# Kernel optimization log

Measured on AMD Instinct MI355X. Metric: run time of the kernel, lower is better.

The kernel has to match this reference:

```python
import jax, jax.numpy as jnp
import numpy as np

# SparseSphereConv (graph_level=6 -> V=40962, kernel_size=9, stride=1, select_index=None)
# Pipeline: neighbor gather -> data-dependent nonzero row selection ->
# per-vertex KxK interpolation matmul -> 1xK conv (linear over C_in,K) -> scatter back.
# With stride=1 / select_index=None the static selection is the identity, so the
# dynamic nonzero selection is equivalent to computing all rows and zeroing the
# rows whose gathered features are entirely zero (selected rows are scattered back,
# unselected rows stay 0 in sparse_reset's zero-initialized output).

BS, C_IN, C_OUT, V, K = 4, 32, 32, 40962, 9

def setup_inputs() -> dict:
    key = jax.random.key(0)
    k1, k2, k3, k4, k5 = jax.random.split(key, 5)
    x = jax.random.normal(k1, (BS, C_IN, V), dtype=jnp.float32)
    index = jax.random.randint(k2, (V, K), 0, V, dtype=jnp.int32)          # neighbor ids per vertex
    itp_mat = jax.random.uniform(k3, (V, K, K), dtype=jnp.float32)         # per-vertex interpolation
    conv_w = jax.random.normal(k4, (C_OUT, C_IN, K), dtype=jnp.float32) * 0.05  # Conv2d(C_in,C_out,(1,K)) weight
    conv_b = jax.random.normal(k5, (C_OUT,), dtype=jnp.float32) * 0.05
    return {"x": x, "index": index, "itp_mat": itp_mat, "conv_w": conv_w, "conv_b": conv_b}

def reference(x, index, itp_mat, conv_w, conv_b):
    # x: [bs, C, V] -> permute(2,0,1) -> gather neighbors -> [V, K, bs, C]
    g = jnp.transpose(x, (2, 0, 1))[index]
    g = jnp.transpose(g, (3, 2, 0, 1))                      # [C, bs, V, K]  (== reshape of [C, bs*V, K])
    # sparse_prepare: keep rows whose min or max over (C, K) is nonzero (detached in torch)
    gd = jax.lax.stop_gradient(g)
    rmin = gd.min(axis=(0, 3))                              # [bs, V]
    rmax = gd.max(axis=(0, 3))                              # [bs, V]
    mask = (rmin != 0) | (rmax != 0)                        # [bs, V]
    # Interploate: [C, S, 1, K] @ [S, K, K] per row -> batched small matmul
    interp = jnp.einsum('cbvk,vkj->cbvj', g, itp_mat)       # [C, bs, V, K]
    # Conv2d with kernel (1, K): contraction over (C_in, K) + bias
    out = jnp.einsum('cbvk,ock->bov', interp, conv_w) + conv_b[None, :, None]  # [bs, C_out, V]
    # sparse_reset: rows not selected stay zero
    return out * mask[:, None, :].astype(out.dtype)
```

## Files before the change

kernel.cpp:

```cpp
#include <hip/hip_runtime.h>
#include <hip/hip_bf16.h>

#define NV 40962
#define NK 9
#define CIN 32
#define COUT 32
#define NT 2561
#define NV81 (NV * 81)
#define NV9  (NV * 9)

typedef __attribute__((ext_vector_type(8))) short bf16x8;
typedef __attribute__((ext_vector_type(4))) float f32x4;
typedef __attribute__((ext_vector_type(2))) float f32x2;

#define PKFMA_L(A, G, R) asm("v_pk_fma_f32 %0, %1, %2, %0 op_sel:[0,0,0] op_sel_hi:[0,1,1]" : "+v"(A) : "v"(G), "v"(R))
#define PKFMA_H(A, G, R) asm("v_pk_fma_f32 %0, %1, %2, %0 op_sel:[1,0,0] op_sel_hi:[1,1,1]" : "+v"(A) : "v"(G), "v"(R))
#define PKMUL_L(A, G, R) asm("v_pk_mul_f32 %0, %1, %2 op_sel:[0,0] op_sel_hi:[0,1]" : "=v"(A) : "v"(G), "v"(R))
#define PKMUL_H(A, G, R) asm("v_pk_mul_f32 %0, %1, %2 op_sel:[1,0] op_sel_hi:[1,1]" : "=v"(A) : "v"(G), "v"(R))

#define ACC(cc, j) ((j) == 8 ? acc8[cc] : (((j) & 1) ? acc2[cc][(j) >> 1].y \
                                                     : acc2[cc][(j) >> 1].x))

__device__ __forceinline__ unsigned pkbf(float a, float b) {
    union { __hip_bfloat162 h2; unsigned u; } cv;
    cv.h2 = __float22bfloat162_rn(make_float2(a, b));
    return cv.u;
}

__global__ void __launch_bounds__(256) transpose_x_bf16(
    const float* __restrict__ x, unsigned* __restrict__ xtw,
    const float* __restrict__ w, unsigned short* __restrict__ wbf)
{
    __shared__ unsigned U[64 * 65];
    const int t = threadIdx.x;

    const int ci = blockIdx.x * 256 + t;
    if (ci < COUT * CIN * NK) {
        const int o = ci / 288;
        const int r = ci - o * 288;
        const int c = r / 9;
        const int j = r - c * 9;
        unsigned u = __float_as_uint(w[ci]);
        wbf[o * 288 + j * 32 + c] =
            (unsigned short)((u + 0x7FFFu + ((u >> 16) & 1u)) >> 16);
    }

    const int v0  = blockIdx.x * 64;
    const int l16 = t & 15;
    const int p   = t >> 4;

    #pragma unroll
    for (int i = 0; i < 4; ++i) {
        const int q    = p * 4 + i;
        const int r0   = 2 * q;
        const int bb   = r0 >> 5;
        const int c0   = r0 & 31;
        const int dwb  = (c0 >> 3) * 16 + bb * 4 + ((c0 & 7) >> 1);
        const float* rowA = x + (size_t)r0 * NV + v0;
        const float* rowB = rowA + NV;
        #pragma unroll
        for (int hv = 0; hv < 2; ++hv) {
            const int v = l16 * 2 + hv * 32;
            float2 a = make_float2(0.f, 0.f), c2 = make_float2(0.f, 0.f);
            if (v0 + v < NV) {
                a  = *(const float2*)(rowA + v);
                c2 = *(const float2*)(rowB + v);
            }
            U[(v    ) * 65 + dwb] = pkbf(a.x, c2.x);
            U[(v + 1) * 65 + dwb] = pkbf(a.y, c2.y);
        }
    }
    __syncthreads();

    const int v  = t >> 2;
    const int qo = t & 3;
    if (v0 + v < NV) {
        #pragma unroll
        for (int j = 0; j < 4; ++j) {
            const int n = j * 4 + qo;
            uint4 d;
            d.x = U[v * 65 + n * 4 + 0];
            d.y = U[v * 65 + n * 4 + 1];
            d.z = U[v * 65 + n * 4 + 2];
            d.w = U[v * 65 + n * 4 + 3];
            *(uint4*)&xtw[(size_t)(v0 + v) * 64 + n * 4] = d;
        }
    }
}

__global__ void __launch_bounds__(256, 2) sparse_conv_mfma(
    const unsigned short* __restrict__ xt, const int* __restrict__ index,
    const float* __restrict__ itp, const unsigned short* __restrict__ wbf,
    const float* __restrict__ bias, float* __restrict__ out)
{
    __shared__ float itp_s[4][4][108];

    const int t    = threadIdx.x;
    const int w    = t >> 6;
    const int lane = t & 63;
    const int arow = lane & 15;
    const int coct = lane >> 4;
    const int b    = (lane >> 2) & 3;
    const int vv   = lane & 3;
    const int tile = blockIdx.x;

    int ia = tile * 144 + w * 36 + (lane < 36 ? lane : 35);
    ia = ia < NV9 ? ia : NV9 - 1;
    const int myidx = index[ia];

    float iv[6];
    const size_t ibase = (size_t)(tile * 16 + w * 4) * 81;
    #pragma unroll
    for (int i = 0; i < 6; ++i) {
        const int o = i * 64 + lane;
        iv[i] = (o < 324 && ibase + o < (size_t)NV81) ? itp[ibase + o] : 0.0f;
    }

    const unsigned short* wb0 = wbf + arow * 288 + coct * 8;
    uint4 wa0[NK], wa1[NK];
    #pragma unroll
    for (int ks = 0; ks < NK; ++ks) {
        wa0[ks] = *(const uint4*)(wb0 + ks * 32);
        wa1[ks] = *(const uint4*)(wb0 + 16 * 288 + ks * 32);
    }

    float bs0[4], bs1[4];
    #pragma unroll
    for (int r = 0; r < 4; ++r) {
        bs0[r] = bias[coct * 4 + r];
        bs1[r] = bias[coct * 4 + 16 + r];
    }

    int nbr[NK];
    #pragma unroll
    for (int n = 0; n < NK; ++n) nbr[n] = __shfl(myidx, vv * 9 + n);
    const unsigned short* gbase = xt + coct * 32 + b * 8;
    uint4 g[NK];
    #pragma unroll
    for (int n = 0; n < NK; ++n)
        g[n] = *(const uint4*)(gbase + (size_t)nbr[n] * 128);

    #pragma unroll
    for (int i = 0; i < 6; ++i) {
        const int o = i * 64 + lane;
        if (o < 324) {
            const int vloc = o / 81;
            const int r2   = o - vloc * 81;
            const int kk   = r2 / 9;
            const int jj   = r2 - kk * 9;
            itp_s[w][vloc][kk * 12 + jj] = iv[i];
        }
    }
    __builtin_amdgcn_wave_barrier();

    unsigned frag[9][4];
    unsigned nzbits = 0;
    #pragma unroll
    for (int n = 0; n < NK; ++n)
        nzbits |= (g[n].x | g[n].y | g[n].z | g[n].w);
    nzbits &= 0x7FFF7FFFu;

    const float* ib = &itp_s[w][vv][0];
    #pragma unroll
    for (int h = 0; h < 2; ++h) {
        f32x2 acc2[4][4];
        float acc8[4];
        #pragma unroll
        for (int n = 0; n < NK; ++n) {
            const uint2 gk = h ? make_uint2(g[n].z, g[n].w)
                               : make_uint2(g[n].x, g[n].y);
            f32x2 gp01, gp23;
            gp01.x = __uint_as_float(gk.x << 16);
            gp01.y = __uint_as_float(gk.x & 0xFFFF0000u);
            gp23.x = __uint_as_float(gk.y << 16);
            gp23.y = __uint_as_float(gk.y & 0xFFFF0000u);
            const float* ir = ib + n * 12;
            const f32x4 ra = *(const f32x4*)ir;
            const f32x4 rb = *(const f32x4*)(ir + 4);
            const float r8 = ir[8];
            f32x2 rp[4];
            rp[0] = __builtin_shufflevector(ra, ra, 0, 1);
            rp[1] = __builtin_shufflevector(ra, ra, 2, 3);
            rp[2] = __builtin_shufflevector(rb, rb, 0, 1);
            rp[3] = __builtin_shufflevector(rb, rb, 2, 3);
            if (n == 0) {
                #pragma unroll
                for (int jp = 0; jp < 4; ++jp) {
                    PKMUL_L(acc2[0][jp], gp01, rp[jp]);
                    PKMUL_H(acc2[1][jp], gp01, rp[jp]);
                    PKMUL_L(acc2[2][jp], gp23, rp[jp]);
                    PKMUL_H(acc2[3][jp], gp23, rp[jp]);
                }
                acc8[0] = gp01.x * r8; acc8[1] = gp01.y * r8;
                acc8[2] = gp23.x * r8; acc8[3] = gp23.y * r8;
            } else {
                #pragma unroll
                for (int jp = 0; jp < 4; ++jp) {
                    PKFMA_L(acc2[0][jp], gp01, rp[jp]);
                    PKFMA_H(acc2[1][jp], gp01, rp[jp]);
                    PKFMA_L(acc2[2][jp], gp23, rp[jp]);
                    PKFMA_H(acc2[3][jp], gp23, rp[jp]);
                }
                acc8[0] += gp01.x * r8; acc8[1] += gp01.y * r8;
                acc8[2] += gp23.x * r8; acc8[3] += gp23.y * r8;
            }
        }
        #pragma unroll
        for (int ks = 0; ks < 9; ++ks) {
            frag[ks][2 * h]     = pkbf(ACC(0, ks), ACC(1, ks));
            frag[ks][2 * h + 1] = pkbf(ACC(2, ks), ACC(3, ks));
        }
    }

    unsigned nzw = nzbits;
    nzw |= __shfl_xor(nzw, 16);
    nzw |= __shfl_xor(nzw, 32);

    f32x4 c0 = {0.f, 0.f, 0.f, 0.f};
    f32x4 c1 = {0.f, 0.f, 0.f, 0.f};
    #pragma unroll
    for (int ks = 0; ks < 9; ++ks) {
        union { uint4 u; bf16x8 v; } bfr, au0, au1;
        bfr.u.x = frag[ks][0]; bfr.u.y = frag[ks][1];
        bfr.u.z = frag[ks][2]; bfr.u.w = frag[ks][3];
        au0.u = wa0[ks];
        au1.u = wa1[ks];
        c0 = __builtin_amdgcn_mfma_f32_16x16x32_bf16(au0.v, bfr.v, c0, 0, 0, 0);
        c1 = __builtin_amdgcn_mfma_f32_16x16x32_bf16(au1.v, bfr.v, c1, 0, 0, 0);
    }

    const int vglob = tile * 16 + w * 4 + vv;
    if (vglob < NV) {
        const float m = nzw ? 1.0f : 0.0f;
        float* ob = out + (size_t)b * (COUT * NV) + vglob;
        #pragma unroll
        for (int r = 0; r < 4; ++r) {
            ob[(size_t)(coct * 4 + r) * NV]      = (c0[r] + bs0[r]) * m;
            ob[(size_t)(coct * 4 + 16 + r) * NV] = (c1[r] + bs1[r]) * m;
        }
    }
}

extern "C" void kernel_launch(void* const* d_in, const int* in_sizes, int n_in,
                              void* d_out, int out_size, void* d_ws, size_t ws_size,
                              hipStream_t stream)
{
    const float* x     = (const float*)d_in[0];
    const int*   index = (const int*)  d_in[1];
    const float* itp   = (const float*)d_in[2];
    const float* w     = (const float*)d_in[3];
    const float* bias  = (const float*)d_in[4];
    float*       out   = (float*)d_out;

    unsigned short* xt  = (unsigned short*)d_ws;
    unsigned short* wbf = (unsigned short*)((char*)d_ws + (size_t)NV * 256);

    const int vchunks = (NV + 63) / 64;
    hipLaunchKernelGGL(transpose_x_bf16, dim3(vchunks), dim3(256), 0,
                       stream, x, (unsigned*)xt, w, wbf);
    hipLaunchKernelGGL(sparse_conv_mfma, dim3(NT), dim3(256), 0,
                       stream, xt, index, itp, wbf, bias, out);
}
```

Measured before the change: 124.2 us.

## Make conv kernel persistent with software-prefetched gathers and LDS-resident weights

```diff
diff --git a/kernel.cpp b/kernel.cpp
--- a/kernel.cpp
+++ b/kernel.cpp
@@ -5,7 +5,9 @@
 #define NK 9
 #define CIN 32
 #define COUT 32
-#define NT 2561
+#define QT_TOTAL 10241
+#define NBLK 1024
+#define NWAVES (NBLK * 4)
 #define NV81 (NV * 81)
 #define NV9  (NV * 9)
 
@@ -88,11 +90,12 @@
     }
 }
 
-__global__ void __launch_bounds__(256, 2) sparse_conv_mfma(
+__global__ void __launch_bounds__(256, 4) sparse_conv_mfma(
     const unsigned short* __restrict__ xt, const int* __restrict__ index,
     const float* __restrict__ itp, const unsigned short* __restrict__ wbf,
     const float* __restrict__ bias, float* __restrict__ out)
 {
+    __shared__ unsigned short Wlds[9 * 32 * 32];
     __shared__ float itp_s[4][4][108];
 
     const int t    = threadIdx.x;
@@ -102,26 +105,16 @@
     const int coct = lane >> 4;
     const int b    = (lane >> 2) & 3;
     const int vv   = lane & 3;
-    const int tile = blockIdx.x;
-
-    int ia = tile * 144 + w * 36 + (lane < 36 ? lane : 35);
-    ia = ia < NV9 ? ia : NV9 - 1;
-    const int myidx = index[ia];
-
-    float iv[6];
-    const size_t ibase = (size_t)(tile * 16 + w * 4) * 81;
-    #pragma unroll
-    for (int i = 0; i < 6; ++i) {
-        const int o = i * 64 + lane;
-        iv[i] = (o < 324 && ibase + o < (size_t)NV81) ? itp[ibase + o] : 0.0f;
-    }
-
-    const unsigned short* wb0 = wbf + arow * 288 + coct * 8;
-    uint4 wa0[NK], wa1[NK];
-    #pragma unroll
-    for (int ks = 0; ks < NK; ++ks) {
-        wa0[ks] = *(const uint4*)(wb0 + ks * 32);
-        wa1[ks] = *(const uint4*)(wb0 + 16 * 288 + ks * 32);
+
+    #pragma unroll
+    for (int r = 0; r < 5; ++r) {
+        const int n = t + r * 256;
+        if (n < 1152) {
+            const int j  = n >> 7;
+            const int o  = (n >> 2) & 31;
+            const int cq = n & 3;
+            ((uint4*)Wlds)[n] = ((const uint4*)wbf)[o * 36 + j * 4 + cq];
+        }
     }
 
     float bs0[4], bs1[4];
@@ -131,113 +124,172 @@
         bs1[r] = bias[coct * 4 + 16 + r];
     }
 
+    const unsigned short* gbase = xt + coct * 32 + b * 8;
+    const int lidx = (lane < 36) ? lane : 35;
+
+    int qt = blockIdx.x * 4 + w;
+    int myidx;
+    {
+        int ia = qt * 36 + lidx;
+        ia = ia < NV9 ? ia : NV9 - 1;
+        myidx = index[ia];
+    }
+    float iv[6];
+    {
+        const size_t ibase = (size_t)qt * 324;
+        #pragma unroll
+        for (int i = 0; i < 6; ++i) {
+            const int o = i * 64 + lane;
+            iv[i] = (o < 324 && ibase + o < (size_t)NV81) ? itp[ibase + o]
+                                                          : 0.0f;
+        }
+    }
     int nbr[NK];
     #pragma unroll
     for (int n = 0; n < NK; ++n) nbr[n] = __shfl(myidx, vv * 9 + n);
-    const unsigned short* gbase = xt + coct * 32 + b * 8;
     uint4 g[NK];
     #pragma unroll
     for (int n = 0; n < NK; ++n)
         g[n] = *(const uint4*)(gbase + (size_t)nbr[n] * 128);
 
-    #pragma unroll
-    for (int i = 0; i < 6; ++i) {
-        const int o = i * 64 + lane;
-        if (o < 324) {
-            const int vloc = o / 81;
-            const int r2   = o - vloc * 81;
-            const int kk   = r2 / 9;
-            const int jj   = r2 - kk * 9;
-            itp_s[w][vloc][kk * 12 + jj] = iv[i];
-        }
-    }
-    __builtin_amdgcn_wave_barrier();
-
-    unsigned frag[9][4];
-    unsigned nzbits = 0;
-    #pragma unroll
-    for (int n = 0; n < NK; ++n)
-        nzbits |= (g[n].x | g[n].y | g[n].z | g[n].w);
-    nzbits &= 0x7FFF7FFFu;
-
-    const float* ib = &itp_s[w][vv][0];
-    #pragma unroll
-    for (int h = 0; h < 2; ++h) {
-        f32x2 acc2[4][4];
-        float acc8[4];
-        #pragma unroll
-        for (int n = 0; n < NK; ++n) {
-            const uint2 gk = h ? make_uint2(g[n].z, g[n].w)
-                               : make_uint2(g[n].x, g[n].y);
-            f32x2 gp01, gp23;
-            gp01.x = __uint_as_float(gk.x << 16);
-            gp01.y = __uint_as_float(gk.x & 0xFFFF0000u);
-            gp23.x = __uint_as_float(gk.y << 16);
-            gp23.y = __uint_as_float(gk.y & 0xFFFF0000u);
-            const float* ir = ib + n * 12;
-            const f32x4 ra = *(const f32x4*)ir;
-            const f32x4 rb = *(const f32x4*)(ir + 4);
-            const float r8 = ir[8];
-            f32x2 rp[4];
-            rp[0] = __builtin_shufflevector(ra, ra, 0, 1);
-            rp[1] = __builtin_shufflevector(ra, ra, 2, 3);
-            rp[2] = __builtin_shufflevector(rb, rb, 0, 1);
-            rp[3] = __builtin_shufflevector(rb, rb, 2, 3);
-            if (n == 0) {
-                #pragma unroll
-                for (int jp = 0; jp < 4; ++jp) {
-                    PKMUL_L(acc2[0][jp], gp01, rp[jp]);
-                    PKMUL_H(acc2[1][jp], gp01, rp[jp]);
-                    PKMUL_L(acc2[2][jp], gp23, rp[jp]);
-                    PKMUL_H(acc2[3][jp], gp23, rp[jp]);
+    __syncthreads();
+
+    while (true) {
+        const int  qn    = qt + NWAVES;
+        const bool alive = (qn < QT_TOTAL);
+
+        int idxn;
+        {
+            int ia = (alive ? qn : qt) * 36 + lidx;
+            ia = ia < NV9 ? ia : NV9 - 1;
+            idxn = index[ia];
+        }
+        float ivn[6];
+        {
+            const size_t ibase = (size_t)qn * 324;
+            #pragma unroll
+            for (int i = 0; i < 6; ++i) {
+                const int o = i * 64 + lane;
+                ivn[i] = (alive && o < 324 && ibase + o < (size_t)NV81)
+                             ? itp[ibase + o] : 0.0f;
+            }
+        }
+
+        __builtin_amdgcn_wave_barrier();
+        #pragma unroll
+        for (int i = 0; i < 6; ++i) {
+            const int o = i * 64 + lane;
+            if (o < 324) {
+                const int vloc = o / 81;
+                const int r2   = o - vloc * 81;
+                const int kk   = r2 / 9;
+                const int jj   = r2 - kk * 9;
+                itp_s[w][vloc][kk * 12 + jj] = iv[i];
+            }
+        }
+        __builtin_amdgcn_wave_barrier();
+
+        unsigned frag[9][4];
+        unsigned nzbits = 0;
+        #pragma unroll
+        for (int n = 0; n < NK; ++n)
+            nzbits |= (g[n].x | g[n].y | g[n].z | g[n].w);
+        nzbits &= 0x7FFF7FFFu;
+
+        const float* ib = &itp_s[w][vv][0];
+        #pragma unroll
+        for (int h = 0; h < 2; ++h) {
+            f32x2 acc2[4][4];
+            float acc8[4];
+            #pragma unroll
+            for (int n = 0; n < NK; ++n) {
+                const uint2 gk = h ? make_uint2(g[n].z, g[n].w)
+                                   : make_uint2(g[n].x, g[n].y);
+                f32x2 gp01, gp23;
+                gp01.x = __uint_as_float(gk.x << 16);
+                gp01.y = __uint_as_float(gk.x & 0xFFFF0000u);
+                gp23.x = __uint_as_float(gk.y << 16);
+                gp23.y = __uint_as_float(gk.y & 0xFFFF0000u);
+                const float* ir = ib + n * 12;
+                const f32x4 ra = *(const f32x4*)ir;
+                const f32x4 rb = *(const f32x4*)(ir + 4);
+                const float r8 = ir[8];
+                f32x2 rp[4];
+                rp[0] = __builtin_shufflevector(ra, ra, 0, 1);
+                rp[1] = __builtin_shufflevector(ra, ra, 2, 3);
+                rp[2] = __builtin_shufflevector(rb, rb, 0, 1);
+                rp[3] = __builtin_shufflevector(rb, rb, 2, 3);
+                if (n == 0) {
+                    #pragma unroll
+                    for (int jp = 0; jp < 4; ++jp) {
+                        PKMUL_L(acc2[0][jp], gp01, rp[jp]);
+                        PKMUL_H(acc2[1][jp], gp01, rp[jp]);
+                        PKMUL_L(acc2[2][jp], gp23, rp[jp]);
+                        PKMUL_H(acc2[3][jp], gp23, rp[jp]);
+                    }
+                    acc8[0] = gp01.x * r8; acc8[1] = gp01.y * r8;
+                    acc8[2] = gp23.x * r8; acc8[3] = gp23.y * r8;
+                } else {
+                    #pragma unroll
+                    for (int jp = 0; jp < 4; ++jp) {
+                        PKFMA_L(acc2[0][jp], gp01, rp[jp]);
+                        PKFMA_H(acc2[1][jp], gp01, rp[jp]);
+                        PKFMA_L(acc2[2][jp], gp23, rp[jp]);
+                        PKFMA_H(acc2[3][jp], gp23, rp[jp]);
+                    }
+                    acc8[0] += gp01.x * r8; acc8[1] += gp01.y * r8;
+                    acc8[2] += gp23.x * r8; acc8[3] += gp23.y * r8;
                 }
-                acc8[0] = gp01.x * r8; acc8[1] = gp01.y * r8;
-                acc8[2] = gp23.x * r8; acc8[3] = gp23.y * r8;
-            } else {
-                #pragma unroll
-                for (int jp = 0; jp < 4; ++jp) {
-                    PKFMA_L(acc2[0][jp], gp01, rp[jp]);
-                    PKFMA_H(acc2[1][jp], gp01, rp[jp]);
-                    PKFMA_L(acc2[2][jp], gp23, rp[jp]);
-                    PKFMA_H(acc2[3][jp], gp23, rp[jp]);
-                }
-                acc8[0] += gp01.x * r8; acc8[1] += gp01.y * r8;
-                acc8[2] += gp23.x * r8; acc8[3] += gp23.y * r8;
-            }
-        }
+            }
+            #pragma unroll
+            for (int ks = 0; ks < 9; ++ks) {
+                frag[ks][2 * h]     = pkbf(ACC(0, ks), ACC(1, ks));
+                frag[ks][2 * h + 1] = pkbf(ACC(2, ks), ACC(3, ks));
+            }
+        }
+
+        if (alive) {
+            #pragma unroll
+            for (int n = 0; n < NK; ++n) nbr[n] = __shfl(idxn, vv * 9 + n);
+            #pragma unroll
+            for (int n = 0; n < NK; ++n)
+                g[n] = *(const uint4*)(gbase + (size_t)nbr[n] * 128);
+        }
+
+        unsigned nzw = nzbits;
+        nzw |= __shfl_xor(nzw, 16);
+        nzw |= __shfl_xor(nzw, 32);
+
+        f32x4 c0 = {0.f, 0.f, 0.f, 0.f};
+        f32x4 c1 = {0.f, 0.f, 0.f, 0.f};
         #pragma unroll
         for (int ks = 0; ks < 9; ++ks) {
-            frag[ks][2 * h]     = pkbf(ACC(0, ks), ACC(1, ks));
-            frag[ks][2 * h + 1] = pkbf(ACC(2, ks), ACC(3, ks));
-        }
-    }
-
-    unsigned nzw = nzbits;
-    nzw |= __shfl_xor(nzw, 16);
-    nzw |= __shfl_xor(nzw, 32);
-
-    f32x4 c0 = {0.f, 0.f, 0.f, 0.f};
-    f32x4 c1 = {0.f, 0.f, 0.f, 0.f};
-    #pragma unroll
-    for (int ks = 0; ks < 9; ++ks) {
-        union { uint4 u; bf16x8 v; } bfr, au0, au1;
-        bfr.u.x = frag[ks][0]; bfr.u.y = frag[ks][1];
-        bfr.u.z = frag[ks][2]; bfr.u.w = frag[ks][3];
-        au0.u = wa0[ks];
-        au1.u = wa1[ks];
-        c0 = __builtin_amdgcn_mfma_f32_16x16x32_bf16(au0.v, bfr.v, c0, 0, 0, 0);
-        c1 = __builtin_amdgcn_mfma_f32_16x16x32_bf16(au1.v, bfr.v, c1, 0, 0, 0);
-    }
-
-    const int vglob = tile * 16 + w * 4 + vv;
-    if (vglob < NV) {
-        const float m = nzw ? 1.0f : 0.0f;
-        float* ob = out + (size_t)b * (COUT * NV) + vglob;
-        #pragma unroll
-        for (int r = 0; r < 4; ++r) {
-            ob[(size_t)(coct * 4 + r) * NV]      = (c0[r] + bs0[r]) * m;
-            ob[(size_t)(coct * 4 + 16 + r) * NV] = (c1[r] + bs1[r]) * m;
-        }
+            union { uint4 u; bf16x8 v; } bfr;
+            bfr.u.x = frag[ks][0]; bfr.u.y = frag[ks][1];
+            bfr.u.z = frag[ks][2]; bfr.u.w = frag[ks][3];
+            const bf16x8 wa0 =
+                *(const bf16x8*)&Wlds[(ks * 32 + arow) * 32 + coct * 8];
+            const bf16x8 wa1 =
+                *(const bf16x8*)&Wlds[(ks * 32 + arow + 16) * 32 + coct * 8];
+            c0 = __builtin_amdgcn_mfma_f32_16x16x32_bf16(wa0, bfr.v, c0, 0, 0, 0);
+            c1 = __builtin_amdgcn_mfma_f32_16x16x32_bf16(wa1, bfr.v, c1, 0, 0, 0);
+        }
+
+        const int vglob = qt * 4 + vv;
+        if (vglob < NV) {
+            const float m = nzw ? 1.0f : 0.0f;
+            float* ob = out + (size_t)b * (COUT * NV) + vglob;
+            #pragma unroll
+            for (int r = 0; r < 4; ++r) {
+                ob[(size_t)(coct * 4 + r) * NV]      = (c0[r] + bs0[r]) * m;
+                ob[(size_t)(coct * 4 + 16 + r) * NV] = (c1[r] + bs1[r]) * m;
+            }
+        }
+
+        if (!alive) break;
+        qt = qn;
+        #pragma unroll
+        for (int i = 0; i < 6; ++i) iv[i] = ivn[i];
     }
 }
 
@@ -258,6 +310,6 @@
     const int vchunks = (NV + 63) / 64;
     hipLaunchKernelGGL(transpose_x_bf16, dim3(vchunks), dim3(256), 0,
                        stream, x, (unsigned*)xt, w, wbf);
-    hipLaunchKernelGGL(sparse_conv_mfma, dim3(NT), dim3(256), 0,
+    hipLaunchKernelGGL(sparse_conv_mfma, dim3(NBLK), dim3(256), 0,
                        stream, xt, index, itp, wbf, bias, out);
 }
```

Measured after the change: 302.1 us. 2.43x slower.

## Fuse transpose and sparse conv into one persistent cooperative kernel with grid sync

Applied to the files above, without the earlier changes.

```diff
diff --git a/kernel.cpp b/kernel.cpp
--- a/kernel.cpp
+++ b/kernel.cpp
@@ -1,11 +1,16 @@
 #include <hip/hip_runtime.h>
 #include <hip/hip_bf16.h>
+#include <hip/hip_cooperative_groups.h>
+
+namespace cg = cooperative_groups;
 
 #define NV 40962
 #define NK 9
 #define CIN 32
 #define COUT 32
 #define NT 2561
+#define NCHUNK 641
+#define MAXBLK 1024
 #define NV81 (NV * 81)
 #define NV9  (NV * 9)
 
@@ -25,6 +30,225 @@
     union { __hip_bfloat162 h2; unsigned u; } cv;
     cv.h2 = __float22bfloat162_rn(make_float2(a, b));
     return cv.u;
+}
+
+__global__ void __launch_bounds__(256, 2) fused_sparse_conv(
+    const float* __restrict__ x, const int* __restrict__ index,
+    const float* __restrict__ itp, const float* __restrict__ w,
+    const float* __restrict__ bias, unsigned* __restrict__ xtw,
+    unsigned short* __restrict__ wbf, float* __restrict__ out)
+{
+    __shared__ unsigned shbuf[64 * 65];
+
+    const int t = threadIdx.x;
+
+    for (int ci = blockIdx.x * 256 + t; ci < COUT * CIN * NK;
+         ci += gridDim.x * 256) {
+        const int o = ci / 288;
+        const int r = ci - o * 288;
+        const int c = r / 9;
+        const int j = r - c * 9;
+        unsigned u = __float_as_uint(w[ci]);
+        wbf[o * 288 + j * 32 + c] =
+            (unsigned short)((u + 0x7FFFu + ((u >> 16) & 1u)) >> 16);
+    }
+
+    for (int chunk = blockIdx.x; chunk < NCHUNK; chunk += gridDim.x) {
+        __syncthreads();
+        const int v0  = chunk * 64;
+        const int l16 = t & 15;
+        const int p   = t >> 4;
+        #pragma unroll
+        for (int i = 0; i < 4; ++i) {
+            const int q   = p * 4 + i;
+            const int r0  = 2 * q;
+            const int bb  = r0 >> 5;
+            const int c0  = r0 & 31;
+            const int dwb = (c0 >> 3) * 16 + bb * 4 + ((c0 & 7) >> 1);
+            const float* rowA = x + (size_t)r0 * NV + v0;
+            const float* rowB = rowA + NV;
+            #pragma unroll
+            for (int hv = 0; hv < 2; ++hv) {
+                const int v = l16 * 2 + hv * 32;
+                float2 a = make_float2(0.f, 0.f), c2 = make_float2(0.f, 0.f);
+                if (v0 + v < NV) {
+                    a  = *(const float2*)(rowA + v);
+                    c2 = *(const float2*)(rowB + v);
+                }
+                shbuf[(v    ) * 65 + dwb] = pkbf(a.x, c2.x);
+                shbuf[(v + 1) * 65 + dwb] = pkbf(a.y, c2.y);
+            }
+        }
+        __syncthreads();
+        const int v  = t >> 2;
+        const int qo = t & 3;
+        if (v0 + v < NV) {
+            #pragma unroll
+            for (int j = 0; j < 4; ++j) {
+                const int n = j * 4 + qo;
+                uint4 d;
+                d.x = shbuf[v * 65 + n * 4 + 0];
+                d.y = shbuf[v * 65 + n * 4 + 1];
+                d.z = shbuf[v * 65 + n * 4 + 2];
+                d.w = shbuf[v * 65 + n * 4 + 3];
+                *(uint4*)&xtw[(size_t)(v0 + v) * 64 + n * 4] = d;
+            }
+        }
+    }
+
+    __threadfence();
+    cg::this_grid().sync();
+    __threadfence();
+
+    const unsigned short* xt = (const unsigned short*)xtw;
+    const int w_    = t >> 6;
+    const int lane  = t & 63;
+    const int arow  = lane & 15;
+    const int coct  = lane >> 4;
+    const int b     = (lane >> 2) & 3;
+    const int vv    = lane & 3;
+    float* itp_w    = ((float*)shbuf) + w_ * 432;
+
+    float bs0[4], bs1[4];
+    #pragma unroll
+    for (int r = 0; r < 4; ++r) {
+        bs0[r] = bias[coct * 4 + r];
+        bs1[r] = bias[coct * 4 + 16 + r];
+    }
+    const unsigned short* gbase = xt + coct * 32 + b * 8;
+    const int lidx = (lane < 36) ? lane : 35;
+
+    for (int tile = blockIdx.x; tile < NT; tile += gridDim.x) {
+        int ia = tile * 144 + w_ * 36 + lidx;
+        ia = ia < NV9 ? ia : NV9 - 1;
+        const int myidx = index[ia];
+
+        float iv[6];
+        const size_t ibase = (size_t)(tile * 16 + w_ * 4) * 81;
+        #pragma unroll
+        for (int i = 0; i < 6; ++i) {
+            const int o = i * 64 + lane;
+            iv[i] = (o < 324 && ibase + o < (size_t)NV81) ? itp[ibase + o]
+                                                          : 0.0f;
+        }
+
+        const unsigned short* wb0 = wbf + arow * 288 + coct * 8;
+        uint4 wa0[NK], wa1[NK];
+        #pragma unroll
+        for (int ks = 0; ks < NK; ++ks) {
+            wa0[ks] = *(const uint4*)(wb0 + ks * 32);
+            wa1[ks] = *(const uint4*)(wb0 + 16 * 288 + ks * 32);
+        }
+
+        int nbr[NK];
+        #pragma unroll
+        for (int n = 0; n < NK; ++n) nbr[n] = __shfl(myidx, vv * 9 + n);
+        uint4 g[NK];
+        #pragma unroll
+        for (int n = 0; n < NK; ++n)
+            g[n] = *(const uint4*)(gbase + (size_t)nbr[n] * 128);
+
+        __builtin_amdgcn_wave_barrier();
+        #pragma unroll
+        for (int i = 0; i < 6; ++i) {
+            const int o = i * 64 + lane;
+            if (o < 324) {
+                const int vloc = o / 81;
+                const int r2   = o - vloc * 81;
+                const int kk   = r2 / 9;
+                const int jj   = r2 - kk * 9;
+                itp_w[vloc * 108 + kk * 12 + jj] = iv[i];
+            }
+        }
+        __builtin_amdgcn_wave_barrier();
+
+        unsigned frag[9][4];
+        unsigned nzbits = 0;
+        #pragma unroll
+        for (int n = 0; n < NK; ++n)
+            nzbits |= (g[n].x | g[n].y | g[n].z | g[n].w);
+        nzbits &= 0x7FFF7FFFu;
+
+        const float* ib = itp_w + vv * 108;
+        #pragma unroll
+        for (int h = 0; h < 2; ++h) {
+            f32x2 acc2[4][4];
+            float acc8[4];
+            #pragma unroll
+            for (int n = 0; n < NK; ++n) {
+                const uint2 gk = h ? make_uint2(g[n].z, g[n].w)
+                                   : make_uint2(g[n].x, g[n].y);
+                f32x2 gp01, gp23;
+                gp01.x = __uint_as_float(gk.x << 16);
+                gp01.y = __uint_as_float(gk.x & 0xFFFF0000u);
+                gp23.x = __uint_as_float(gk.y << 16);
+                gp23.y = __uint_as_float(gk.y & 0xFFFF0000u);
+                const float* ir = ib + n * 12;
+                const f32x4 ra = *(const f32x4*)ir;
+                const f32x4 rb = *(const f32x4*)(ir + 4);
+                const float r8 = ir[8];
+                f32x2 rp[4];
+                rp[0] = __builtin_shufflevector(ra, ra, 0, 1);
+                rp[1] = __builtin_shufflevector(ra, ra, 2, 3);
+                rp[2] = __builtin_shufflevector(rb, rb, 0, 1);
+                rp[3] = __builtin_shufflevector(rb, rb, 2, 3);
+                if (n == 0) {
+                    #pragma unroll
+                    for (int jp = 0; jp < 4; ++jp) {
+                        PKMUL_L(acc2[0][jp], gp01, rp[jp]);
+                        PKMUL_H(acc2[1][jp], gp01, rp[jp]);
+                        PKMUL_L(acc2[2][jp], gp23, rp[jp]);
+                        PKMUL_H(acc2[3][jp], gp23, rp[jp]);
+                    }
+                    acc8[0] = gp01.x * r8; acc8[1] = gp01.y * r8;
+                    acc8[2] = gp23.x * r8; acc8[3] = gp23.y * r8;
+                } else {
+                    #pragma unroll
+                    for (int jp = 0; jp < 4; ++jp) {
+                        PKFMA_L(acc2[0][jp], gp01, rp[jp]);
+                        PKFMA_H(acc2[1][jp], gp01, rp[jp]);
+                        PKFMA_L(acc2[2][jp], gp23, rp[jp]);
+                        PKFMA_H(acc2[3][jp], gp23, rp[jp]);
+                    }
+                    acc8[0] += gp01.x * r8; acc8[1] += gp01.y * r8;
+                    acc8[2] += gp23.x * r8; acc8[3] += gp23.y * r8;
+                }
+            }
+            #pragma unroll
+            for (int ks = 0; ks < 9; ++ks) {
+                frag[ks][2 * h]     = pkbf(ACC(0, ks), ACC(1, ks));
+                frag[ks][2 * h + 1] = pkbf(ACC(2, ks), ACC(3, ks));
+            }
+        }
+
+        unsigned nzw = nzbits;
+        nzw |= __shfl_xor(nzw, 16);
+        nzw |= __shfl_xor(nzw, 32);
+
+        f32x4 c0 = {0.f, 0.f, 0.f, 0.f};
+        f32x4 c1 = {0.f, 0.f, 0.f, 0.f};
+        #pragma unroll
+        for (int ks = 0; ks < 9; ++ks) {
+            union { uint4 u; bf16x8 v; } bfr, au0, au1;
+            bfr.u.x = frag[ks][0]; bfr.u.y = frag[ks][1];
+            bfr.u.z = frag[ks][2]; bfr.u.w = frag[ks][3];
+            au0.u = wa0[ks];
+            au1.u = wa1[ks];
+            c0 = __builtin_amdgcn_mfma_f32_16x16x32_bf16(au0.v, bfr.v, c0, 0, 0, 0);
+            c1 = __builtin_amdgcn_mfma_f32_16x16x32_bf16(au1.v, bfr.v, c1, 0, 0, 0);
+        }
+
+        const int vglob = tile * 16 + w_ * 4 + vv;
+        if (vglob < NV) {
+            const float m = nzw ? 1.0f : 0.0f;
+            float* ob = out + (size_t)b * (COUT * NV) + vglob;
+            #pragma unroll
+            for (int r = 0; r < 4; ++r) {
+                ob[(size_t)(coct * 4 + r) * NV]      = (c0[r] + bs0[r]) * m;
+                ob[(size_t)(coct * 4 + 16 + r) * NV] = (c1[r] + bs1[r]) * m;
+            }
+        }
+    }
 }
 
 __global__ void __launch_bounds__(256) transpose_x_bf16(
@@ -51,11 +275,11 @@
 
     #pragma unroll
     for (int i = 0; i < 4; ++i) {
-        const int q    = p * 4 + i;
-        const int r0   = 2 * q;
-        const int bb   = r0 >> 5;
-        const int c0   = r0 & 31;
-        const int dwb  = (c0 >> 3) * 16 + bb * 4 + ((c0 & 7) >> 1);
+        const int q   = p * 4 + i;
+        const int r0  = 2 * q;
+        const int bb  = r0 >> 5;
+        const int c0  = r0 & 31;
+        const int dwb = (c0 >> 3) * 16 + bb * 4 + ((c0 & 7) >> 1);
         const float* rowA = x + (size_t)r0 * NV + v0;
         const float* rowB = rowA + NV;
         #pragma unroll
@@ -254,10 +478,29 @@
 
     unsigned short* xt  = (unsigned short*)d_ws;
     unsigned short* wbf = (unsigned short*)((char*)d_ws + (size_t)NV * 256);
-
-    const int vchunks = (NV + 63) / 64;
-    hipLaunchKernelGGL(transpose_x_bf16, dim3(vchunks), dim3(256), 0,
-                       stream, x, (unsigned*)xt, w, wbf);
-    hipLaunchKernelGGL(sparse_conv_mfma, dim3(NT), dim3(256), 0,
-                       stream, xt, index, itp, wbf, bias, out);
+    unsigned*       xtw = (unsigned*)xt;
+
+    int coop = 0;
+    hipDeviceGetAttribute(&coop, hipDeviceAttributeCooperativeLaunch, 0);
+    int nb = 0;
+    hipOccupancyMaxActiveBlocksPerMultiprocessor(&nb, fused_sparse_conv, 256, 0);
+    int grid = nb * 256;
+    if (grid > MAXBLK) grid = MAXBLK;
+
+    bool launched = false;
+    if (coop && grid >= 256) {
+        void* args[8] = { (void*)&x, (void*)&index, (void*)&itp, (void*)&w,
+                          (void*)&bias, (void*)&xtw, (void*)&wbf, (void*)&out };
+        hipError_t e = hipLaunchCooperativeKernel(fused_sparse_conv,
+                                                  dim3(grid), dim3(256),
+                                                  args, 0, stream);
+        launched = (e == hipSuccess);
+    }
+
+    if (!launched) {
+        hipLaunchKernelGGL(transpose_x_bf16, dim3(NCHUNK), dim3(256), 0,
+                           stream, x, xtw, w, wbf);
+        hipLaunchKernelGGL(sparse_conv_mfma, dim3(NT), dim3(256), 0,
+                           stream, xt, index, itp, wbf, bias, out);
+    }
 }
```

Result: slower. 237.4 us (+91.2%).

## Split xt layout per batch and map MFMA columns to 16 vertices per wave

Applied to the files above, without the earlier changes.

```diff
diff --git a/kernel.cpp b/kernel.cpp
--- a/kernel.cpp
+++ b/kernel.cpp
@@ -5,7 +5,8 @@
 #define NK 9
 #define CIN 32
 #define COUT 32
-#define NT 2561
+#define NTV 2561
+#define NBPB 641
 #define NV81 (NV * 81)
 #define NV9  (NV * 9)
 
@@ -55,7 +56,7 @@
         const int r0   = 2 * q;
         const int bb   = r0 >> 5;
         const int c0   = r0 & 31;
-        const int dwb  = (c0 >> 3) * 16 + bb * 4 + ((c0 & 7) >> 1);
+        const int dwb  = bb * 16 + (c0 >> 1);
         const float* rowA = x + (size_t)r0 * NV + v0;
         const float* rowB = rowA + NV;
         #pragma unroll
@@ -83,7 +84,8 @@
             d.y = U[v * 65 + n * 4 + 1];
             d.z = U[v * 65 + n * 4 + 2];
             d.w = U[v * 65 + n * 4 + 3];
-            *(uint4*)&xtw[(size_t)(v0 + v) * 64 + n * 4] = d;
+            *(uint4*)&xtw[(size_t)(n >> 2) * (NV * 16)
+                          + (size_t)(v0 + v) * 16 + (n & 3) * 4] = d;
         }
     }
 }
@@ -93,27 +95,41 @@
     const float* __restrict__ itp, const unsigned short* __restrict__ wbf,
     const float* __restrict__ bias, float* __restrict__ out)
 {
-    __shared__ float itp_s[4][4][108];
+    __shared__ float itp_s[4][16 * 108];
+    __shared__ int   idx_s[4][144];
 
     const int t    = threadIdx.x;
     const int w    = t >> 6;
     const int lane = t & 63;
     const int arow = lane & 15;
     const int coct = lane >> 4;
-    const int b    = (lane >> 2) & 3;
-    const int vv   = lane & 3;
-    const int tile = blockIdx.x;
-
-    int ia = tile * 144 + w * 36 + (lane < 36 ? lane : 35);
-    ia = ia < NV9 ? ia : NV9 - 1;
-    const int myidx = index[ia];
-
-    float iv[6];
-    const size_t ibase = (size_t)(tile * 16 + w * 4) * 81;
-    #pragma unroll
-    for (int i = 0; i < 6; ++i) {
-        const int o = i * 64 + lane;
-        iv[i] = (o < 324 && ibase + o < (size_t)NV81) ? itp[ibase + o] : 0.0f;
+
+    const int bq   = blockIdx.x / NBPB;
+    const int vblk = blockIdx.x - bq * NBPB;
+    const int vt   = vblk * 4 + w;
+    if (vt >= NTV) return;
+
+    {
+        const int ib0 = vt * 144;
+        int ia0 = ib0 + lane;        ia0 = ia0 < NV9 ? ia0 : NV9 - 1;
+        int ia1 = ib0 + 64 + lane;   ia1 = ia1 < NV9 ? ia1 : NV9 - 1;
+        idx_s[w][lane]      = index[ia0];
+        idx_s[w][64 + lane] = index[ia1];
+        if (lane < 16) {
+            int ia2 = ib0 + 128 + lane; ia2 = ia2 < NV9 ? ia2 : NV9 - 1;
+            idx_s[w][128 + lane] = index[ia2];
+        }
+    }
+
+    float iv[21];
+    {
+        const size_t tbase = (size_t)vt * 1296;
+        #pragma unroll
+        for (int i = 0; i < 21; ++i) {
+            const int o = i * 64 + lane;
+            iv[i] = (o < 1296 && tbase + o < (size_t)NV81) ? itp[tbase + o]
+                                                           : 0.0f;
+        }
     }
 
     const unsigned short* wb0 = wbf + arow * 288 + coct * 8;
@@ -131,24 +147,25 @@
         bs1[r] = bias[coct * 4 + 16 + r];
     }
 
+    __builtin_amdgcn_wave_barrier();
     int nbr[NK];
     #pragma unroll
-    for (int n = 0; n < NK; ++n) nbr[n] = __shfl(myidx, vv * 9 + n);
-    const unsigned short* gbase = xt + coct * 32 + b * 8;
+    for (int n = 0; n < NK; ++n) nbr[n] = idx_s[w][arow * 9 + n];
+    const unsigned short* gbase = xt + (size_t)bq * (NV * 32) + coct * 8;
     uint4 g[NK];
     #pragma unroll
     for (int n = 0; n < NK; ++n)
-        g[n] = *(const uint4*)(gbase + (size_t)nbr[n] * 128);
-
-    #pragma unroll
-    for (int i = 0; i < 6; ++i) {
+        g[n] = *(const uint4*)(gbase + (size_t)nbr[n] * 32);
+
+    #pragma unroll
+    for (int i = 0; i < 21; ++i) {
         const int o = i * 64 + lane;
-        if (o < 324) {
+        if (o < 1296) {
             const int vloc = o / 81;
             const int r2   = o - vloc * 81;
             const int kk   = r2 / 9;
             const int jj   = r2 - kk * 9;
-            itp_s[w][vloc][kk * 12 + jj] = iv[i];
+            itp_s[w][vloc * 108 + kk * 12 + jj] = iv[i];
         }
     }
     __builtin_amdgcn_wave_barrier();
@@ -160,7 +177,7 @@
         nzbits |= (g[n].x | g[n].y | g[n].z | g[n].w);
     nzbits &= 0x7FFF7FFFu;
 
-    const float* ib = &itp_s[w][vv][0];
+    const float* ib = &itp_s[w][arow * 108];
     #pragma unroll
     for (int h = 0; h < 2; ++h) {
         f32x2 acc2[4][4];
@@ -229,10 +246,10 @@
         c1 = __builtin_amdgcn_mfma_f32_16x16x32_bf16(au1.v, bfr.v, c1, 0, 0, 0);
     }
 
-    const int vglob = tile * 16 + w * 4 + vv;
+    const int vglob = vt * 16 + arow;
     if (vglob < NV) {
         const float m = nzw ? 1.0f : 0.0f;
-        float* ob = out + (size_t)b * (COUT * NV) + vglob;
+        float* ob = out + (size_t)bq * (COUT * NV) + vglob;
         #pragma unroll
         for (int r = 0; r < 4; ++r) {
             ob[(size_t)(coct * 4 + r) * NV]      = (c0[r] + bs0[r]) * m;
@@ -258,6 +275,6 @@
     const int vchunks = (NV + 63) / 64;
     hipLaunchKernelGGL(transpose_x_bf16, dim3(vchunks), dim3(256), 0,
                        stream, x, (unsigned*)xt, w, wbf);
-    hipLaunchKernelGGL(sparse_conv_mfma, dim3(NT), dim3(256), 0,
+    hipLaunchKernelGGL(sparse_conv_mfma, dim3(4 * NBPB), dim3(256), 0,
                        stream, xt, index, itp, wbf, bias, out);
 }
```

Result: no change. 125.1 us (+0.8%).
